# Kernel optimization log

Hardware: AMD Instinct MI355X
Metric: run time of the kernel (lower is better)

The kernel has to match this reference:

```python
import jax, jax.numpy as jnp
import numpy as np

B, S, HID, H, HKV, HD = 2, 1024, 4096, 32, 8, 128
NEG = -1e9
W_STD = 0.02


def _rotary(q, k, pos):
    # NeoX-style rotate-half rotary embedding, theta=10000
    inv_freq = 1.0 / (10000.0 ** (jnp.arange(0, HD, 2, dtype=jnp.float32) / HD))  # [HD/2]
    ang = pos[..., None].astype(jnp.float32) * inv_freq            # [B,S,HD/2]
    cos = jnp.concatenate([jnp.cos(ang), jnp.cos(ang)], -1)[:, :, None, :]  # [B,S,1,HD]
    sin = jnp.concatenate([jnp.sin(ang), jnp.sin(ang)], -1)[:, :, None, :]

    def rot_half(t):
        h1, h2 = jnp.split(t, 2, axis=-1)
        return jnp.concatenate([-h2, h1], axis=-1)

    return q * cos + rot_half(q) * sin, k * cos + rot_half(k) * sin


def setup_inputs() -> dict:
    key = jax.random.key(0)
    ks = jax.random.split(key, 6)
    x = jax.random.normal(ks[0], (B * S, HID), jnp.float32)
    wq = jax.random.normal(ks[1], (HID, H * HD), jnp.float32) * W_STD
    wk = jax.random.normal(ks[2], (HID, HKV * HD), jnp.float32) * W_STD
    wv = jax.random.normal(ks[3], (HID, HKV * HD), jnp.float32) * W_STD
    wo = jax.random.normal(ks[4], (H * HD, HID), jnp.float32) * W_STD
    # additive causal mask (module uses is_causal=False and an explicit attn_mask)
    attn_mask = jnp.where(jnp.triu(jnp.ones((S, S), bool), 1), NEG, 0.0).astype(jnp.float32)
    return {
        "x": x,
        "attn_mask": attn_mask,
        "wq": wq, "wk": wk, "wv": wv, "wo": wo,
        "seqstarts": jnp.arange(B + 1, dtype=jnp.int32) * S,
        "kvstarts": jnp.arange(B + 1, dtype=jnp.int32) * S,
        "cachestarts": jnp.arange(B, dtype=jnp.int32) * S,
        "decoding_batches": 0,
        "start_pos": jnp.zeros((B,), jnp.int32),
        "max_seqlen": S,
        "max_kvlen": S,
        "first_seqlen": jnp.full((B,), S, jnp.int32),
        "kv_cache": jnp.zeros((1,), jnp.float32),
        "kv_scale": jnp.zeros((1,), jnp.float32),
    }


def reference(x, attn_mask, wq, wk, wv, wo, seqstarts, kvstarts, cachestarts,
              decoding_batches, start_pos, max_seqlen, max_kvlen, first_seqlen,
              kv_cache, kv_scale):
    # QKV projections on flattened ragged tokens (uniform seqlens -> dense [B,S])
    xq = (x @ wq).reshape(B, S, H, HD)
    xk = (x @ wk).reshape(B, S, HKV, HD)
    xv = (x @ wv).reshape(B, S, HKV, HD)
    pos = start_pos[:, None] + jnp.arange(S, dtype=jnp.int32)  # [B,S]
    xq, xk = _rotary(xq, xk, pos)
    # GQA: repeat kv heads (friendly_gqa path of key_value_cache, num_repeat=4)
    g = H // HKV
    k = jnp.repeat(xk, g, axis=2)  # [B,S,H,HD]
    v = jnp.repeat(xv, g, axis=2)
    scale = 1.0 / jnp.sqrt(jnp.float32(HD))
    scores = jnp.einsum('bqhd,bkhd->bhqk', xq, k) * scale + attn_mask  # [B,H,S,S]
    p = jax.nn.softmax(scores, axis=-1)
    attn = jnp.einsum('bhqk,bkhd->bqhd', p, v).reshape(B * S, H * HD)
    return attn @ wo
```

## Files before the change

kernel.cpp:

```cpp
#include <hip/hip_runtime.h>
#include <hip/hip_bf16.h>

#define B_    2
#define S_    1024
#define HID_  4096
#define H_    32
#define HKV_  8
#define HD_   128

typedef __attribute__((ext_vector_type(8))) short   bf16x8_t;
typedef __attribute__((ext_vector_type(4))) float   f32x4_t;

__device__ __forceinline__ unsigned short f2bf(float f) {
    union { float f; unsigned u; } v; v.f = f;
    unsigned r = v.u + 0x7fffu + ((v.u >> 16) & 1u);
    return (unsigned short)(r >> 16);
}
__device__ __forceinline__ float bf2f(unsigned short u) {
    union { unsigned u; float f; } v; v.u = ((unsigned)u) << 16;
    return v.f;
}

__device__ __forceinline__ void gload_lds16(const void* g, void* l) {
    __builtin_amdgcn_global_load_lds(
        (const __attribute__((address_space(1))) unsigned int*)g,
        (__attribute__((address_space(3))) unsigned int*)l, 16, 0, 0);
}

__global__ __launch_bounds__(256) void cvt_f32_bf16(const float* __restrict__ in,
                                                    unsigned short* __restrict__ out,
                                                    int n4) {
    int i = blockIdx.x * 256 + threadIdx.x;
    if (i >= n4) return;
    float4 v = reinterpret_cast<const float4*>(in)[i];
    uint2 p;
    p.x = (unsigned)f2bf(v.x) | ((unsigned)f2bf(v.y) << 16);
    p.y = (unsigned)f2bf(v.z) | ((unsigned)f2bf(v.w) << 16);
    reinterpret_cast<uint2*>(out)[i] = p;
}

__global__ __launch_bounds__(256) void tcvt(const float* __restrict__ W,
                                            unsigned short* __restrict__ Wt,
                                            int ldW, int Kdim) {
    __shared__ unsigned short L[32][36];
    const int t = threadIdx.x;
    const int kb = blockIdx.y, nb = blockIdx.x;
    {
        int kr = t >> 3, nc = (t & 7) * 4;
        float4 v = *reinterpret_cast<const float4*>(&W[(size_t)(kb * 32 + kr) * ldW + nb * 32 + nc]);
        L[nc + 0][kr] = f2bf(v.x);
        L[nc + 1][kr] = f2bf(v.y);
        L[nc + 2][kr] = f2bf(v.z);
        L[nc + 3][kr] = f2bf(v.w);
    }
    __syncthreads();
    {
        int nr = t >> 3, kc = (t & 7) * 4;
        uint2 o;
        o.x = (unsigned)L[nr][kc + 0] | ((unsigned)L[nr][kc + 1] << 16);
        o.y = (unsigned)L[nr][kc + 2] | ((unsigned)L[nr][kc + 3] << 16);
        *reinterpret_cast<uint2*>(&Wt[(size_t)(nb * 32 + nr) * Kdim + kb * 32 + kc]) = o;
    }
}

template<bool OUT_BF16>
__global__ __launch_bounds__(256) void gemm_tt(
    const unsigned short* __restrict__ A,
    const unsigned short* __restrict__ Bt,
    void* __restrict__ Cm,
    int ldc, int K)
{
    __shared__ unsigned short As[2][128 * 32];
    __shared__ unsigned short Bs[2][128 * 32];
    const int tid  = threadIdx.x;
    const int lane = tid & 63;
    const int w    = tid >> 6;
    const int wm   = w >> 1, wn = w & 1;
    const int r    = lane & 15, g = lane >> 4;

    const int nwg = gridDim.x * gridDim.y;
    const int D   = blockIdx.y * gridDim.x + blockIdx.x;
    const int L   = (D & 7) * (nwg >> 3) + (D >> 3);
    const int m0  = (L / gridDim.x) * 128, n0 = (L % gridDim.x) * 128;

    const int c0 = w * 128 + lane;
    const int c1 = c0 + 64;
    const int r0 = c0 >> 2, col0 = (((c0 & 3) ^ (r0 & 3)) << 3);
    const int r1 = c1 >> 2, col1 = (((c1 & 3) ^ (r1 & 3)) << 3);
    const int sw = (g ^ (r & 3)) << 3;

    const f32x4_t zero = {0.f, 0.f, 0.f, 0.f};
    f32x4_t acc[4][4];
#pragma unroll
    for (int i = 0; i < 4; ++i)
#pragma unroll
        for (int j = 0; j < 4; ++j) acc[i][j] = zero;

    gload_lds16(&A [(size_t)(m0 + r0) * K + col0], &As[0][(w * 2 + 0) * 512]);
    gload_lds16(&A [(size_t)(m0 + r1) * K + col1], &As[0][(w * 2 + 1) * 512]);
    gload_lds16(&Bt[(size_t)(n0 + r0) * K + col0], &Bs[0][(w * 2 + 0) * 512]);
    gload_lds16(&Bt[(size_t)(n0 + r1) * K + col1], &Bs[0][(w * 2 + 1) * 512]);
    __syncthreads();

    int cur = 0;
    for (int k0 = 0; k0 < K; k0 += 32) {
        if (k0 + 32 < K) {
            const int nk = k0 + 32, nb = cur ^ 1;
            gload_lds16(&A [(size_t)(m0 + r0) * K + nk + col0], &As[nb][(w * 2 + 0) * 512]);
            gload_lds16(&A [(size_t)(m0 + r1) * K + nk + col1], &As[nb][(w * 2 + 1) * 512]);
            gload_lds16(&Bt[(size_t)(n0 + r0) * K + nk + col0], &Bs[nb][(w * 2 + 0) * 512]);
            gload_lds16(&Bt[(size_t)(n0 + r1) * K + nk + col1], &Bs[nb][(w * 2 + 1) * 512]);
        }
        bf16x8_t af[4], bfr[4];
#pragma unroll
        for (int m = 0; m < 4; ++m)
            af[m] = *reinterpret_cast<const bf16x8_t*>(&As[cur][(wm * 64 + m * 16 + r) * 32 + sw]);
#pragma unroll
        for (int n = 0; n < 4; ++n)
            bfr[n] = *reinterpret_cast<const bf16x8_t*>(&Bs[cur][(wn * 64 + n * 16 + r) * 32 + sw]);
#pragma unroll
        for (int m = 0; m < 4; ++m)
#pragma unroll
            for (int n = 0; n < 4; ++n)
                acc[m][n] = __builtin_amdgcn_mfma_f32_16x16x32_bf16(af[m], bfr[n], acc[m][n], 0, 0, 0);
        __syncthreads();
        cur ^= 1;
    }

#pragma unroll
    for (int m = 0; m < 4; ++m)
#pragma unroll
        for (int n = 0; n < 4; ++n)
#pragma unroll
            for (int j = 0; j < 4; ++j) {
                int row = m0 + wm * 64 + m * 16 + g * 4 + j;
                int col = n0 + wn * 64 + n * 16 + r;
                if constexpr (OUT_BF16)
                    reinterpret_cast<unsigned short*>(Cm)[(size_t)row * ldc + col] = f2bf(acc[m][n][j]);
                else
                    reinterpret_cast<float*>(Cm)[(size_t)row * ldc + col] = acc[m][n][j];
            }
}

__global__ __launch_bounds__(256) void gemm_qkv(
    const unsigned short* __restrict__ A,
    const unsigned short* __restrict__ BtQ,
    const unsigned short* __restrict__ BtKV,
    unsigned short* __restrict__ Qb,
    unsigned short* __restrict__ Kb,
    unsigned short* __restrict__ VT,
    int K)
{
    __shared__ unsigned short As[2][128 * 32];
    __shared__ unsigned short Bs[2][128 * 32];
    const int tid  = threadIdx.x;
    const int lane = tid & 63;
    const int w    = tid >> 6;
    const int wm   = w >> 1, wn = w & 1;
    const int r    = lane & 15, g = lane >> 4;

    const int nwg = gridDim.x * gridDim.y;
    const int D   = blockIdx.y * gridDim.x + blockIdx.x;
    const int L   = (D & 7) * (nwg >> 3) + (D >> 3);
    const int m0  = (L / gridDim.x) * 128, n0 = (L % gridDim.x) * 128;

    const unsigned short* Brow = (n0 < 4096) ? (BtQ + (size_t)n0 * K)
                                             : (BtKV + (size_t)(n0 - 4096) * K);

    const int c0 = w * 128 + lane;
    const int c1 = c0 + 64;
    const int r0 = c0 >> 2, col0 = (((c0 & 3) ^ (r0 & 3)) << 3);
    const int r1 = c1 >> 2, col1 = (((c1 & 3) ^ (r1 & 3)) << 3);
    const int sw = (g ^ (r & 3)) << 3;

    const f32x4_t zero = {0.f, 0.f, 0.f, 0.f};
    f32x4_t acc[4][4];
#pragma unroll
    for (int i = 0; i < 4; ++i)
#pragma unroll
        for (int j = 0; j < 4; ++j) acc[i][j] = zero;

    gload_lds16(&A   [(size_t)(m0 + r0) * K + col0], &As[0][(w * 2 + 0) * 512]);
    gload_lds16(&A   [(size_t)(m0 + r1) * K + col1], &As[0][(w * 2 + 1) * 512]);
    gload_lds16(&Brow[(size_t)r0 * K + col0],        &Bs[0][(w * 2 + 0) * 512]);
    gload_lds16(&Brow[(size_t)r1 * K + col1],        &Bs[0][(w * 2 + 1) * 512]);
    __syncthreads();

    int cur = 0;
    for (int k0 = 0; k0 < K; k0 += 32) {
        if (k0 + 32 < K) {
            const int nk = k0 + 32, nb = cur ^ 1;
            gload_lds16(&A   [(size_t)(m0 + r0) * K + nk + col0], &As[nb][(w * 2 + 0) * 512]);
            gload_lds16(&A   [(size_t)(m0 + r1) * K + nk + col1], &As[nb][(w * 2 + 1) * 512]);
            gload_lds16(&Brow[(size_t)r0 * K + nk + col0],        &Bs[nb][(w * 2 + 0) * 512]);
            gload_lds16(&Brow[(size_t)r1 * K + nk + col1],        &Bs[nb][(w * 2 + 1) * 512]);
        }
        bf16x8_t af[4], bfr[4];
#pragma unroll
        for (int m = 0; m < 4; ++m)
            af[m] = *reinterpret_cast<const bf16x8_t*>(&As[cur][(wm * 64 + m * 16 + r) * 32 + sw]);
#pragma unroll
        for (int n = 0; n < 4; ++n)
            bfr[n] = *reinterpret_cast<const bf16x8_t*>(&Bs[cur][(wn * 64 + n * 16 + r) * 32 + sw]);
#pragma unroll
        for (int m = 0; m < 4; ++m)
#pragma unroll
            for (int n = 0; n < 4; ++n)
                acc[m][n] = __builtin_amdgcn_mfma_f32_16x16x32_bf16(af[m], bfr[n], acc[m][n], 0, 0, 0);
        __syncthreads();
        cur ^= 1;
    }

#pragma unroll
    for (int m = 0; m < 4; ++m)
#pragma unroll
        for (int n = 0; n < 4; ++n) {
            int col  = n0 + wn * 64 + n * 16 + r;
            int row0 = m0 + wm * 64 + m * 16 + g * 4;
            if (n0 < 4096) {
#pragma unroll
                for (int j = 0; j < 4; ++j)
                    Qb[(size_t)(row0 + j) * 4096 + col] = f2bf(acc[m][n][j]);
            } else if (n0 < 5120) {
#pragma unroll
                for (int j = 0; j < 4; ++j)
                    Kb[(size_t)(row0 + j) * 1024 + (col - 4096)] = f2bf(acc[m][n][j]);
            } else {
                int d = col - 5120;
                int b = row0 >> 10, tokl = row0 & 1023;
                uint2 o;
                o.x = (unsigned)f2bf(acc[m][n][0]) | ((unsigned)f2bf(acc[m][n][1]) << 16);
                o.y = (unsigned)f2bf(acc[m][n][2]) | ((unsigned)f2bf(acc[m][n][3]) << 16);
                *reinterpret_cast<uint2*>(&VT[(size_t)(b * 1024 + d) * 1024 + tokl]) = o;
            }
        }
}

__global__ __launch_bounds__(256) void rope_table_kernel(const int* __restrict__ start_pos,
                                                         float* __restrict__ tab) {
    int i = blockIdx.x * 256 + threadIdx.x;
    int d = i & 63;
    int tok = i >> 6;
    int s = tok & (S_ - 1);
    int b = tok >> 10;
    float pos = (float)(start_pos[b] + s);
    float freq = __expf(-(float)d * (9.210340371976184f / 64.f));
    float ang = pos * freq;
    tab[tok * 128 + d]      = cosf(ang);
    tab[tok * 128 + 64 + d] = sinf(ang);
}

template<int LOGH, int STRIDE>
__global__ __launch_bounds__(256) void rope_apply_kernel(unsigned short* __restrict__ t,
                                                         const float* __restrict__ tab) {
    int i = blockIdx.x * 256 + threadIdx.x;
    int d = i & 63;
    int h = (i >> 6) & ((1 << LOGH) - 1);
    int tok = i >> (6 + LOGH);
    size_t base = (size_t)tok * STRIDE + (size_t)h * 128;
    float c  = tab[tok * 128 + d];
    float sn = tab[tok * 128 + 64 + d];
    float a = bf2f(t[base + d]);
    float b = bf2f(t[base + 64 + d]);
    t[base + d]      = f2bf(a * c - b * sn);
    t[base + 64 + d] = f2bf(b * c + a * sn);
}

__global__ __launch_bounds__(64) void attn_fwd(
    const unsigned short* __restrict__ Qb,
    const unsigned short* __restrict__ Kb,
    const unsigned short* __restrict__ VT,
    unsigned short* __restrict__ Ob)
{
    const int nQT = S_ / 32;
    const int qt = nQT - 1 - blockIdx.y;
    const int h = blockIdx.x, b = blockIdx.z;
    const int kvh = h >> 2;
    const int lane = threadIdx.x;
    const int r = lane & 15, g = lane >> 4;
    __shared__ unsigned short P_lds[32][40];

    const int qrow0 = qt * 32;
    const unsigned short* Qp = Qb + ((size_t)(b * S_) + qrow0) * 4096 + h * 128;
    bf16x8_t qf[2][4];
#pragma unroll
    for (int q2 = 0; q2 < 2; ++q2)
#pragma unroll
        for (int kk = 0; kk < 4; ++kk)
            qf[q2][kk] = *reinterpret_cast<const bf16x8_t*>(
                &Qp[(size_t)(q2 * 16 + r) * 4096 + kk * 32 + g * 8]);

    const f32x4_t zero = {0.f, 0.f, 0.f, 0.f};
    f32x4_t o[2][8];
#pragma unroll
    for (int q2 = 0; q2 < 2; ++q2)
#pragma unroll
        for (int n = 0; n < 8; ++n) o[q2][n] = zero;
    float m_[2][4], s_[2][4];
#pragma unroll
    for (int q2 = 0; q2 < 2; ++q2)
#pragma unroll
        for (int j = 0; j < 4; ++j) { m_[q2][j] = -1e30f; s_[q2][j] = 0.f; }

    const float scale = 0.08838834764831845f;
    const unsigned short* Kp = Kb + (size_t)(b * S_) * 1024 + kvh * 128;
    const unsigned short* Vt = VT + ((size_t)(b * 1024) + kvh * 128) * 1024;
    const int ntiles = qt + 1;

    for (int t = 0; t < ntiles; ++t) {
        const int k0 = t << 5;
        f32x4_t sc[2][2];
        sc[0][0] = zero; sc[0][1] = zero; sc[1][0] = zero; sc[1][1] = zero;
        __builtin_amdgcn_s_setprio(1);
#pragma unroll
        for (int kk = 0; kk < 4; ++kk) {
            bf16x8_t kf0 = *reinterpret_cast<const bf16x8_t*>(
                &Kp[(size_t)(k0 + r) * 1024 + kk * 32 + g * 8]);
            bf16x8_t kf1 = *reinterpret_cast<const bf16x8_t*>(
                &Kp[(size_t)(k0 + 16 + r) * 1024 + kk * 32 + g * 8]);
#pragma unroll
            for (int q2 = 0; q2 < 2; ++q2) {
                sc[q2][0] = __builtin_amdgcn_mfma_f32_16x16x32_bf16(qf[q2][kk], kf0, sc[q2][0], 0, 0, 0);
                sc[q2][1] = __builtin_amdgcn_mfma_f32_16x16x32_bf16(qf[q2][kk], kf1, sc[q2][1], 0, 0, 0);
            }
        }
        __builtin_amdgcn_s_setprio(0);
        bf16x8_t vf[8];
#pragma unroll
        for (int n = 0; n < 8; ++n)
            vf[n] = *reinterpret_cast<const bf16x8_t*>(
                &Vt[(size_t)(n * 16 + r) * 1024 + k0 + g * 8]);
        float al[2][4];
#pragma unroll
        for (int q2 = 0; q2 < 2; ++q2)
#pragma unroll
            for (int j = 0; j < 4; ++j) {
                int row = qrow0 + q2 * 16 + g * 4 + j;
                float v0 = sc[q2][0][j] * scale + ((k0 + r)      > row ? -1e9f : 0.f);
                float v1 = sc[q2][1][j] * scale + ((k0 + 16 + r) > row ? -1e9f : 0.f);
                float mx = fmaxf(v0, v1);
#pragma unroll
                for (int off = 1; off < 16; off <<= 1)
                    mx = fmaxf(mx, __shfl_xor(mx, off));
                float mn = fmaxf(m_[q2][j], mx);
                al[q2][j] = __expf(m_[q2][j] - mn);
                float p0 = __expf(v0 - mn);
                float p1 = __expf(v1 - mn);
                float rs = p0 + p1;
#pragma unroll
                for (int off = 1; off < 16; off <<= 1)
                    rs += __shfl_xor(rs, off);
                s_[q2][j] = s_[q2][j] * al[q2][j] + rs;
                m_[q2][j] = mn;
                P_lds[q2 * 16 + g * 4 + j][r]      = f2bf(p0);
                P_lds[q2 * 16 + g * 4 + j][16 + r] = f2bf(p1);
            }
#pragma unroll
        for (int q2 = 0; q2 < 2; ++q2)
#pragma unroll
            for (int n = 0; n < 8; ++n)
#pragma unroll
                for (int j = 0; j < 4; ++j)
                    o[q2][n][j] *= al[q2][j];
        __syncthreads();
        bf16x8_t pa[2];
        pa[0] = *reinterpret_cast<const bf16x8_t*>(&P_lds[r][g * 8]);
        pa[1] = *reinterpret_cast<const bf16x8_t*>(&P_lds[16 + r][g * 8]);
        __builtin_amdgcn_s_setprio(1);
#pragma unroll
        for (int n = 0; n < 8; ++n)
#pragma unroll
            for (int q2 = 0; q2 < 2; ++q2)
                o[q2][n] = __builtin_amdgcn_mfma_f32_16x16x32_bf16(pa[q2], vf[n], o[q2][n], 0, 0, 0);
        __builtin_amdgcn_s_setprio(0);
        __syncthreads();
    }
    unsigned short* Op = Ob + ((size_t)(b * S_) + qrow0) * 4096 + h * 128;
#pragma unroll
    for (int q2 = 0; q2 < 2; ++q2)
#pragma unroll
        for (int n = 0; n < 8; ++n)
#pragma unroll
            for (int j = 0; j < 4; ++j) {
                float val = o[q2][n][j] / s_[q2][j];
                Op[(size_t)(q2 * 16 + g * 4 + j) * 4096 + n * 16 + r] = f2bf(val);
            }
}

extern "C" void kernel_launch(void* const* d_in, const int* in_sizes, int n_in,
                              void* d_out, int out_size, void* d_ws, size_t ws_size,
                              hipStream_t stream)
{
    const float* x  = (const float*)d_in[0];
    const float* wq = (const float*)d_in[2];
    const float* wk = (const float*)d_in[3];
    const float* wv = (const float*)d_in[4];
    const float* wo = (const float*)d_in[5];
    const int* start_pos = (const int*)d_in[10];

    char* ws = (char*)d_ws;
    unsigned short* xb   = (unsigned short*)(ws);
    unsigned short* qb   = (unsigned short*)(ws + (16u << 20));
    unsigned short* kb   = (unsigned short*)(ws + (32u << 20));
    unsigned short* vT   = (unsigned short*)(ws + (36u << 20));
    unsigned short* wkvT = (unsigned short*)(ws + (40u << 20));
    float*          tb   = (float*)(ws + (56u << 20));
    unsigned short* ab   = xb;
    unsigned short* wqT  = (unsigned short*)d_out;
    unsigned short* woT  = qb;

    cvt_f32_bf16<<<8192, 256, 0, stream>>>(x, xb, (B_ * S_ * HID_) / 4);

    tcvt<<<dim3(128, 128), 256, 0, stream>>>(wq, wqT, HID_, HID_);
    tcvt<<<dim3(32, 128), 256, 0, stream>>>(wk, wkvT, 1024, HID_);
    tcvt<<<dim3(32, 128), 256, 0, stream>>>(wv, wkvT + (size_t)1024 * HID_, 1024, HID_);

    gemm_qkv<<<dim3(48, 16), 256, 0, stream>>>(xb, wqT, wkvT, qb, kb, vT, HID_);

    rope_table_kernel<<<512, 256, 0, stream>>>(start_pos, tb);
    rope_apply_kernel<5, 4096><<<16384, 256, 0, stream>>>(qb, tb);
    rope_apply_kernel<3, 1024><<<4096, 256, 0, stream>>>(kb, tb);

    attn_fwd<<<dim3(H_, S_ / 32, B_), 64, 0, stream>>>(qb, kb, vT, ab);

    tcvt<<<dim3(128, 128), 256, 0, stream>>>(wo, woT, HID_, HID_);
    gemm_tt<false><<<dim3(32, 16), 256, 0, stream>>>(ab, woT, (float*)d_out, 4096, HID_);
}
```

Measured before the change: 566.8 us.

## Fuse prep conversions, fold RoPE into QKV epilogue, merge attention with wo transpose

```diff
diff --git a/kernel.cpp b/kernel.cpp
--- a/kernel.cpp
+++ b/kernel.cpp
@@ -27,24 +27,10 @@
         (__attribute__((address_space(3))) unsigned int*)l, 16, 0, 0);
 }
 
-__global__ __launch_bounds__(256) void cvt_f32_bf16(const float* __restrict__ in,
-                                                    unsigned short* __restrict__ out,
-                                                    int n4) {
-    int i = blockIdx.x * 256 + threadIdx.x;
-    if (i >= n4) return;
-    float4 v = reinterpret_cast<const float4*>(in)[i];
-    uint2 p;
-    p.x = (unsigned)f2bf(v.x) | ((unsigned)f2bf(v.y) << 16);
-    p.y = (unsigned)f2bf(v.z) | ((unsigned)f2bf(v.w) << 16);
-    reinterpret_cast<uint2*>(out)[i] = p;
-}
-
-__global__ __launch_bounds__(256) void tcvt(const float* __restrict__ W,
-                                            unsigned short* __restrict__ Wt,
-                                            int ldW, int Kdim) {
-    __shared__ unsigned short L[32][36];
-    const int t = threadIdx.x;
-    const int kb = blockIdx.y, nb = blockIdx.x;
+__device__ __forceinline__ void tcvt_body(const float* __restrict__ W,
+                                          unsigned short* __restrict__ Wt,
+                                          int ldW, int nb, int kb,
+                                          unsigned short (*L)[36], int t) {
     {
         int kr = t >> 3, nc = (t & 7) * 4;
         float4 v = *reinterpret_cast<const float4*>(&W[(size_t)(kb * 32 + kr) * ldW + nb * 32 + nc]);
@@ -59,15 +45,300 @@
         uint2 o;
         o.x = (unsigned)L[nr][kc + 0] | ((unsigned)L[nr][kc + 1] << 16);
         o.y = (unsigned)L[nr][kc + 2] | ((unsigned)L[nr][kc + 3] << 16);
-        *reinterpret_cast<uint2*>(&Wt[(size_t)(nb * 32 + nr) * Kdim + kb * 32 + kc]) = o;
-    }
-}
-
-template<bool OUT_BF16>
+        *reinterpret_cast<uint2*>(&Wt[(size_t)(nb * 32 + nr) * 4096 + kb * 32 + kc]) = o;
+    }
+}
+
+__global__ __launch_bounds__(256) void prep(
+    const float* __restrict__ x,  const float* __restrict__ wq,
+    const float* __restrict__ wk, const float* __restrict__ wv,
+    const int* __restrict__ start_pos,
+    unsigned short* __restrict__ xb, unsigned short* __restrict__ wqT,
+    unsigned short* __restrict__ wkvT, float* __restrict__ tb)
+{
+    const int bid = blockIdx.x;
+    const int t   = threadIdx.x;
+    if (bid < 8192) {
+        int i = bid * 256 + t;
+        float4 v = reinterpret_cast<const float4*>(x)[i];
+        uint2 p;
+        p.x = (unsigned)f2bf(v.x) | ((unsigned)f2bf(v.y) << 16);
+        p.y = (unsigned)f2bf(v.z) | ((unsigned)f2bf(v.w) << 16);
+        reinterpret_cast<uint2*>(xb)[i] = p;
+        return;
+    }
+    if (bid >= 32768) {
+        int i = (bid - 32768) * 256 + t;
+        int d = i & 63;
+        int tok = i >> 6;
+        int s = tok & (S_ - 1);
+        int b = tok >> 10;
+        float pos = (float)(start_pos[b] + s);
+        float freq = __expf(-(float)d * (9.210340371976184f / 64.f));
+        float ang = pos * freq;
+        tb[tok * 128 + d]      = cosf(ang);
+        tb[tok * 128 + 64 + d] = sinf(ang);
+        return;
+    }
+    __shared__ unsigned short L[32][36];
+    if (bid < 24576) {
+        int q = bid - 8192;
+        tcvt_body(wq, wqT, 4096, q & 127, q >> 7, L, t);
+    } else if (bid < 28672) {
+        int q = bid - 24576;
+        tcvt_body(wk, wkvT, 1024, q & 31, q >> 5, L, t);
+    } else {
+        int q = bid - 28672;
+        tcvt_body(wv, wkvT + (size_t)1024 * 4096, 1024, q & 31, q >> 5, L, t);
+    }
+}
+
+__global__ __launch_bounds__(256) void gemm_qkv(
+    const unsigned short* __restrict__ A,
+    const unsigned short* __restrict__ BtQ,
+    const unsigned short* __restrict__ BtKV,
+    const float* __restrict__ tb,
+    unsigned short* __restrict__ Qb,
+    unsigned short* __restrict__ Kb,
+    unsigned short* __restrict__ VT,
+    int K)
+{
+    __shared__ unsigned short LDS[16384];
+    unsigned short* As0 = LDS;
+    unsigned short* Bs0 = LDS + 8192;
+    const int tid  = threadIdx.x;
+    const int lane = tid & 63;
+    const int w    = tid >> 6;
+    const int wm   = w >> 1, wn = w & 1;
+    const int r    = lane & 15, g = lane >> 4;
+
+    const int nwg = gridDim.x * gridDim.y;
+    const int D   = blockIdx.y * gridDim.x + blockIdx.x;
+    const int L   = (D & 7) * (nwg >> 3) + (D >> 3);
+    const int m0  = (L / gridDim.x) * 128, n0 = (L % gridDim.x) * 128;
+
+    const unsigned short* Brow = (n0 < 4096) ? (BtQ + (size_t)n0 * K)
+                                             : (BtKV + (size_t)(n0 - 4096) * K);
+
+    const int c0 = w * 128 + lane;
+    const int c1 = c0 + 64;
+    const int r0 = c0 >> 2, col0 = (((c0 & 3) ^ (r0 & 3)) << 3);
+    const int r1 = c1 >> 2, col1 = (((c1 & 3) ^ (r1 & 3)) << 3);
+    const int sw = (g ^ (r & 3)) << 3;
+
+    const f32x4_t zero = {0.f, 0.f, 0.f, 0.f};
+    f32x4_t acc[4][4];
+#pragma unroll
+    for (int i = 0; i < 4; ++i)
+#pragma unroll
+        for (int j = 0; j < 4; ++j) acc[i][j] = zero;
+
+    gload_lds16(&A   [(size_t)(m0 + r0) * K + col0], &As0[(w * 2 + 0) * 512]);
+    gload_lds16(&A   [(size_t)(m0 + r1) * K + col1], &As0[(w * 2 + 1) * 512]);
+    gload_lds16(&Brow[(size_t)r0 * K + col0],        &Bs0[(w * 2 + 0) * 512]);
+    gload_lds16(&Brow[(size_t)r1 * K + col1],        &Bs0[(w * 2 + 1) * 512]);
+    __syncthreads();
+
+    int cur = 0;
+    for (int k0 = 0; k0 < K; k0 += 32) {
+        if (k0 + 32 < K) {
+            const int nk = k0 + 32, nb = cur ^ 1;
+            gload_lds16(&A   [(size_t)(m0 + r0) * K + nk + col0], &As0[nb * 4096 + (w * 2 + 0) * 512]);
+            gload_lds16(&A   [(size_t)(m0 + r1) * K + nk + col1], &As0[nb * 4096 + (w * 2 + 1) * 512]);
+            gload_lds16(&Brow[(size_t)r0 * K + nk + col0],        &Bs0[nb * 4096 + (w * 2 + 0) * 512]);
+            gload_lds16(&Brow[(size_t)r1 * K + nk + col1],        &Bs0[nb * 4096 + (w * 2 + 1) * 512]);
+        }
+        bf16x8_t af[4], bfr[4];
+#pragma unroll
+        for (int m = 0; m < 4; ++m)
+            af[m] = *reinterpret_cast<const bf16x8_t*>(&As0[cur * 4096 + (wm * 64 + m * 16 + r) * 32 + sw]);
+#pragma unroll
+        for (int n = 0; n < 4; ++n)
+            bfr[n] = *reinterpret_cast<const bf16x8_t*>(&Bs0[cur * 4096 + (wn * 64 + n * 16 + r) * 32 + sw]);
+#pragma unroll
+        for (int m = 0; m < 4; ++m)
+#pragma unroll
+            for (int n = 0; n < 4; ++n)
+                acc[m][n] = __builtin_amdgcn_mfma_f32_16x16x32_bf16(af[m], bfr[n], acc[m][n], 0, 0, 0);
+        __syncthreads();
+        cur ^= 1;
+    }
+
+    if (n0 < 5120) {
+#pragma unroll
+        for (int m = 0; m < 4; ++m)
+#pragma unroll
+            for (int n = 0; n < 4; ++n)
+#pragma unroll
+                for (int j = 0; j < 4; ++j)
+                    LDS[(wm * 64 + m * 16 + g * 4 + j) * 128 + wn * 64 + n * 16 + r] = f2bf(acc[m][n][j]);
+        __syncthreads();
+        unsigned short* dst; int ldd, coff;
+        if (n0 < 4096) { dst = Qb; ldd = 4096; coff = n0; }
+        else           { dst = Kb; ldd = 1024; coff = n0 - 4096; }
+        for (int i = tid; i < 8192; i += 256) {
+            int row = i >> 6, dlo = i & 63;
+            int tok = m0 + row;
+            float a  = bf2f(LDS[row * 128 + dlo]);
+            float b  = bf2f(LDS[row * 128 + 64 + dlo]);
+            float c  = tb[tok * 128 + dlo];
+            float sn = tb[tok * 128 + 64 + dlo];
+            dst[(size_t)tok * ldd + coff + dlo]      = f2bf(a * c - b * sn);
+            dst[(size_t)tok * ldd + coff + 64 + dlo] = f2bf(b * c + a * sn);
+        }
+    } else {
+#pragma unroll
+        for (int m = 0; m < 4; ++m)
+#pragma unroll
+            for (int n = 0; n < 4; ++n) {
+                int col  = n0 + wn * 64 + n * 16 + r;
+                int row0 = m0 + wm * 64 + m * 16 + g * 4;
+                int d = col - 5120;
+                int b = row0 >> 10, tokl = row0 & 1023;
+                uint2 o;
+                o.x = (unsigned)f2bf(acc[m][n][0]) | ((unsigned)f2bf(acc[m][n][1]) << 16);
+                o.y = (unsigned)f2bf(acc[m][n][2]) | ((unsigned)f2bf(acc[m][n][3]) << 16);
+                *reinterpret_cast<uint2*>(&VT[(size_t)(b * 1024 + d) * 1024 + tokl]) = o;
+            }
+    }
+}
+
+__global__ __launch_bounds__(256) void attn_tcvt(
+    unsigned short* __restrict__ Qb,
+    const unsigned short* __restrict__ Kb,
+    const unsigned short* __restrict__ VT,
+    const float* __restrict__ wo,
+    unsigned short* __restrict__ woT)
+{
+    const int bid = blockIdx.x;
+    const int tid = threadIdx.x;
+    __shared__ unsigned short P_lds[4][32][40];
+    __shared__ unsigned short Lt[32][36];
+
+    if (bid >= 512) {
+        int q = bid - 512;
+        tcvt_body(wo, woT, 4096, q & 127, q >> 7, Lt, tid);
+        return;
+    }
+
+    const int wid  = tid >> 6;
+    const int lane = tid & 63;
+    const int h    = bid & 31;
+    const int tmp  = bid >> 5;
+    const int qtg  = tmp & 7;
+    const int b    = tmp >> 3;
+    const int qt   = 31 - (qtg + wid * 8);
+    const int kvh  = h >> 2;
+    const int r = lane & 15, g = lane >> 4;
+
+    const int qrow0 = qt * 32;
+    unsigned short* Qp = Qb + ((size_t)(b * S_) + qrow0) * 4096 + h * 128;
+    bf16x8_t qf[2][4];
+#pragma unroll
+    for (int q2 = 0; q2 < 2; ++q2)
+#pragma unroll
+        for (int kk = 0; kk < 4; ++kk)
+            qf[q2][kk] = *reinterpret_cast<const bf16x8_t*>(
+                &Qp[(size_t)(q2 * 16 + r) * 4096 + kk * 32 + g * 8]);
+
+    const f32x4_t zero = {0.f, 0.f, 0.f, 0.f};
+    f32x4_t o[2][8];
+#pragma unroll
+    for (int q2 = 0; q2 < 2; ++q2)
+#pragma unroll
+        for (int n = 0; n < 8; ++n) o[q2][n] = zero;
+    float m_[2][4], s_[2][4];
+#pragma unroll
+    for (int q2 = 0; q2 < 2; ++q2)
+#pragma unroll
+        for (int j = 0; j < 4; ++j) { m_[q2][j] = -1e30f; s_[q2][j] = 0.f; }
+
+    const float scale = 0.08838834764831845f;
+    const unsigned short* Kp = Kb + (size_t)(b * S_) * 1024 + kvh * 128;
+    const unsigned short* Vt = VT + ((size_t)(b * 1024) + kvh * 128) * 1024;
+    const int ntiles = qt + 1;
+
+    for (int t = 0; t < ntiles; ++t) {
+        const int k0 = t << 5;
+        f32x4_t sc[2][2];
+        sc[0][0] = zero; sc[0][1] = zero; sc[1][0] = zero; sc[1][1] = zero;
+        __builtin_amdgcn_s_setprio(1);
+#pragma unroll
+        for (int kk = 0; kk < 4; ++kk) {
+            bf16x8_t kf0 = *reinterpret_cast<const bf16x8_t*>(
+                &Kp[(size_t)(k0 + r) * 1024 + kk * 32 + g * 8]);
+            bf16x8_t kf1 = *reinterpret_cast<const bf16x8_t*>(
+                &Kp[(size_t)(k0 + 16 + r) * 1024 + kk * 32 + g * 8]);
+#pragma unroll
+            for (int q2 = 0; q2 < 2; ++q2) {
+                sc[q2][0] = __builtin_amdgcn_mfma_f32_16x16x32_bf16(qf[q2][kk], kf0, sc[q2][0], 0, 0, 0);
+                sc[q2][1] = __builtin_amdgcn_mfma_f32_16x16x32_bf16(qf[q2][kk], kf1, sc[q2][1], 0, 0, 0);
+            }
+        }
+        __builtin_amdgcn_s_setprio(0);
+        bf16x8_t vf[8];
+#pragma unroll
+        for (int n = 0; n < 8; ++n)
+            vf[n] = *reinterpret_cast<const bf16x8_t*>(
+                &Vt[(size_t)(n * 16 + r) * 1024 + k0 + g * 8]);
+        float al[2][4];
+#pragma unroll
+        for (int q2 = 0; q2 < 2; ++q2)
+#pragma unroll
+            for (int j = 0; j < 4; ++j) {
+                int row = qrow0 + q2 * 16 + g * 4 + j;
+                float v0 = sc[q2][0][j] * scale + ((k0 + r)      > row ? -1e9f : 0.f);
+                float v1 = sc[q2][1][j] * scale + ((k0 + 16 + r) > row ? -1e9f : 0.f);
+                float mx = fmaxf(v0, v1);
+#pragma unroll
+                for (int off = 1; off < 16; off <<= 1)
+                    mx = fmaxf(mx, __shfl_xor(mx, off));
+                float mn = fmaxf(m_[q2][j], mx);
+                al[q2][j] = __expf(m_[q2][j] - mn);
+                float p0 = __expf(v0 - mn);
+                float p1 = __expf(v1 - mn);
+                float rs = p0 + p1;
+#pragma unroll
+                for (int off = 1; off < 16; off <<= 1)
+                    rs += __shfl_xor(rs, off);
+                s_[q2][j] = s_[q2][j] * al[q2][j] + rs;
+                m_[q2][j] = mn;
+                P_lds[wid][q2 * 16 + g * 4 + j][r]      = f2bf(p0);
+                P_lds[wid][q2 * 16 + g * 4 + j][16 + r] = f2bf(p1);
+            }
+#pragma unroll
+        for (int q2 = 0; q2 < 2; ++q2)
+#pragma unroll
+            for (int n = 0; n < 8; ++n)
+#pragma unroll
+                for (int j = 0; j < 4; ++j)
+                    o[q2][n][j] *= al[q2][j];
+        bf16x8_t pa[2];
+        pa[0] = *reinterpret_cast<const bf16x8_t*>(&P_lds[wid][r][g * 8]);
+        pa[1] = *reinterpret_cast<const bf16x8_t*>(&P_lds[wid][16 + r][g * 8]);
+        __builtin_amdgcn_s_setprio(1);
+#pragma unroll
+        for (int n = 0; n < 8; ++n)
+#pragma unroll
+            for (int q2 = 0; q2 < 2; ++q2)
+                o[q2][n] = __builtin_amdgcn_mfma_f32_16x16x32_bf16(pa[q2], vf[n], o[q2][n], 0, 0, 0);
+        __builtin_amdgcn_s_setprio(0);
+    }
+#pragma unroll
+    for (int q2 = 0; q2 < 2; ++q2)
+#pragma unroll
+        for (int n = 0; n < 8; ++n)
+#pragma unroll
+            for (int j = 0; j < 4; ++j) {
+                float val = o[q2][n][j] / s_[q2][j];
+                Qp[(size_t)(q2 * 16 + g * 4 + j) * 4096 + n * 16 + r] = f2bf(val);
+            }
+}
+
 __global__ __launch_bounds__(256) void gemm_tt(
     const unsigned short* __restrict__ A,
     const unsigned short* __restrict__ Bt,
-    void* __restrict__ Cm,
+    float* __restrict__ Cm,
     int ldc, int K)
 {
     __shared__ unsigned short As[2][128 * 32];
@@ -135,255 +406,7 @@
             for (int j = 0; j < 4; ++j) {
                 int row = m0 + wm * 64 + m * 16 + g * 4 + j;
                 int col = n0 + wn * 64 + n * 16 + r;
-                if constexpr (OUT_BF16)
-                    reinterpret_cast<unsigned short*>(Cm)[(size_t)row * ldc + col] = f2bf(acc[m][n][j]);
-                else
-                    reinterpret_cast<float*>(Cm)[(size_t)row * ldc + col] = acc[m][n][j];
-            }
-}
-
-__global__ __launch_bounds__(256) void gemm_qkv(
-    const unsigned short* __restrict__ A,
-    const unsigned short* __restrict__ BtQ,
-    const unsigned short* __restrict__ BtKV,
-    unsigned short* __restrict__ Qb,
-    unsigned short* __restrict__ Kb,
-    unsigned short* __restrict__ VT,
-    int K)
-{
-    __shared__ unsigned short As[2][128 * 32];
-    __shared__ unsigned short Bs[2][128 * 32];
-    const int tid  = threadIdx.x;
-    const int lane = tid & 63;
-    const int w    = tid >> 6;
-    const int wm   = w >> 1, wn = w & 1;
-    const int r    = lane & 15, g = lane >> 4;
-
-    const int nwg = gridDim.x * gridDim.y;
-    const int D   = blockIdx.y * gridDim.x + blockIdx.x;
-    const int L   = (D & 7) * (nwg >> 3) + (D >> 3);
-    const int m0  = (L / gridDim.x) * 128, n0 = (L % gridDim.x) * 128;
-
-    const unsigned short* Brow = (n0 < 4096) ? (BtQ + (size_t)n0 * K)
-                                             : (BtKV + (size_t)(n0 - 4096) * K);
-
-    const int c0 = w * 128 + lane;
-    const int c1 = c0 + 64;
-    const int r0 = c0 >> 2, col0 = (((c0 & 3) ^ (r0 & 3)) << 3);
-    const int r1 = c1 >> 2, col1 = (((c1 & 3) ^ (r1 & 3)) << 3);
-    const int sw = (g ^ (r & 3)) << 3;
-
-    const f32x4_t zero = {0.f, 0.f, 0.f, 0.f};
-    f32x4_t acc[4][4];
-#pragma unroll
-    for (int i = 0; i < 4; ++i)
-#pragma unroll
-        for (int j = 0; j < 4; ++j) acc[i][j] = zero;
-
-    gload_lds16(&A   [(size_t)(m0 + r0) * K + col0], &As[0][(w * 2 + 0) * 512]);
-    gload_lds16(&A   [(size_t)(m0 + r1) * K + col1], &As[0][(w * 2 + 1) * 512]);
-    gload_lds16(&Brow[(size_t)r0 * K + col0],        &Bs[0][(w * 2 + 0) * 512]);
-    gload_lds16(&Brow[(size_t)r1 * K + col1],        &Bs[0][(w * 2 + 1) * 512]);
-    __syncthreads();
-
-    int cur = 0;
-    for (int k0 = 0; k0 < K; k0 += 32) {
-        if (k0 + 32 < K) {
-            const int nk = k0 + 32, nb = cur ^ 1;
-            gload_lds16(&A   [(size_t)(m0 + r0) * K + nk + col0], &As[nb][(w * 2 + 0) * 512]);
-            gload_lds16(&A   [(size_t)(m0 + r1) * K + nk + col1], &As[nb][(w * 2 + 1) * 512]);
-            gload_lds16(&Brow[(size_t)r0 * K + nk + col0],        &Bs[nb][(w * 2 + 0) * 512]);
-            gload_lds16(&Brow[(size_t)r1 * K + nk + col1],        &Bs[nb][(w * 2 + 1) * 512]);
-        }
-        bf16x8_t af[4], bfr[4];
-#pragma unroll
-        for (int m = 0; m < 4; ++m)
-            af[m] = *reinterpret_cast<const bf16x8_t*>(&As[cur][(wm * 64 + m * 16 + r) * 32 + sw]);
-#pragma unroll
-        for (int n = 0; n < 4; ++n)
-            bfr[n] = *reinterpret_cast<const bf16x8_t*>(&Bs[cur][(wn * 64 + n * 16 + r) * 32 + sw]);
-#pragma unroll
-        for (int m = 0; m < 4; ++m)
-#pragma unroll
-            for (int n = 0; n < 4; ++n)
-                acc[m][n] = __builtin_amdgcn_mfma_f32_16x16x32_bf16(af[m], bfr[n], acc[m][n], 0, 0, 0);
-        __syncthreads();
-        cur ^= 1;
-    }
-
-#pragma unroll
-    for (int m = 0; m < 4; ++m)
-#pragma unroll
-        for (int n = 0; n < 4; ++n) {
-            int col  = n0 + wn * 64 + n * 16 + r;
-            int row0 = m0 + wm * 64 + m * 16 + g * 4;
-            if (n0 < 4096) {
-#pragma unroll
-                for (int j = 0; j < 4; ++j)
-                    Qb[(size_t)(row0 + j) * 4096 + col] = f2bf(acc[m][n][j]);
-            } else if (n0 < 5120) {
-#pragma unroll
-                for (int j = 0; j < 4; ++j)
-                    Kb[(size_t)(row0 + j) * 1024 + (col - 4096)] = f2bf(acc[m][n][j]);
-            } else {
-                int d = col - 5120;
-                int b = row0 >> 10, tokl = row0 & 1023;
-                uint2 o;
-                o.x = (unsigned)f2bf(acc[m][n][0]) | ((unsigned)f2bf(acc[m][n][1]) << 16);
-                o.y = (unsigned)f2bf(acc[m][n][2]) | ((unsigned)f2bf(acc[m][n][3]) << 16);
-                *reinterpret_cast<uint2*>(&VT[(size_t)(b * 1024 + d) * 1024 + tokl]) = o;
-            }
-        }
-}
-
-__global__ __launch_bounds__(256) void rope_table_kernel(const int* __restrict__ start_pos,
-                                                         float* __restrict__ tab) {
-    int i = blockIdx.x * 256 + threadIdx.x;
-    int d = i & 63;
-    int tok = i >> 6;
-    int s = tok & (S_ - 1);
-    int b = tok >> 10;
-    float pos = (float)(start_pos[b] + s);
-    float freq = __expf(-(float)d * (9.210340371976184f / 64.f));
-    float ang = pos * freq;
-    tab[tok * 128 + d]      = cosf(ang);
-    tab[tok * 128 + 64 + d] = sinf(ang);
-}
-
-template<int LOGH, int STRIDE>
-__global__ __launch_bounds__(256) void rope_apply_kernel(unsigned short* __restrict__ t,
-                                                         const float* __restrict__ tab) {
-    int i = blockIdx.x * 256 + threadIdx.x;
-    int d = i & 63;
-    int h = (i >> 6) & ((1 << LOGH) - 1);
-    int tok = i >> (6 + LOGH);
-    size_t base = (size_t)tok * STRIDE + (size_t)h * 128;
-    float c  = tab[tok * 128 + d];
-    float sn = tab[tok * 128 + 64 + d];
-    float a = bf2f(t[base + d]);
-    float b = bf2f(t[base + 64 + d]);
-    t[base + d]      = f2bf(a * c - b * sn);
-    t[base + 64 + d] = f2bf(b * c + a * sn);
-}
-
-__global__ __launch_bounds__(64) void attn_fwd(
-    const unsigned short* __restrict__ Qb,
-    const unsigned short* __restrict__ Kb,
-    const unsigned short* __restrict__ VT,
-    unsigned short* __restrict__ Ob)
-{
-    const int nQT = S_ / 32;
-    const int qt = nQT - 1 - blockIdx.y;
-    const int h = blockIdx.x, b = blockIdx.z;
-    const int kvh = h >> 2;
-    const int lane = threadIdx.x;
-    const int r = lane & 15, g = lane >> 4;
-    __shared__ unsigned short P_lds[32][40];
-
-    const int qrow0 = qt * 32;
-    const unsigned short* Qp = Qb + ((size_t)(b * S_) + qrow0) * 4096 + h * 128;
-    bf16x8_t qf[2][4];
-#pragma unroll
-    for (int q2 = 0; q2 < 2; ++q2)
-#pragma unroll
-        for (int kk = 0; kk < 4; ++kk)
-            qf[q2][kk] = *reinterpret_cast<const bf16x8_t*>(
-                &Qp[(size_t)(q2 * 16 + r) * 4096 + kk * 32 + g * 8]);
-
-    const f32x4_t zero = {0.f, 0.f, 0.f, 0.f};
-    f32x4_t o[2][8];
-#pragma unroll
-    for (int q2 = 0; q2 < 2; ++q2)
-#pragma unroll
-        for (int n = 0; n < 8; ++n) o[q2][n] = zero;
-    float m_[2][4], s_[2][4];
-#pragma unroll
-    for (int q2 = 0; q2 < 2; ++q2)
-#pragma unroll
-        for (int j = 0; j < 4; ++j) { m_[q2][j] = -1e30f; s_[q2][j] = 0.f; }
-
-    const float scale = 0.08838834764831845f;
-    const unsigned short* Kp = Kb + (size_t)(b * S_) * 1024 + kvh * 128;
-    const unsigned short* Vt = VT + ((size_t)(b * 1024) + kvh * 128) * 1024;
-    const int ntiles = qt + 1;
-
-    for (int t = 0; t < ntiles; ++t) {
-        const int k0 = t << 5;
-        f32x4_t sc[2][2];
-        sc[0][0] = zero; sc[0][1] = zero; sc[1][0] = zero; sc[1][1] = zero;
-        __builtin_amdgcn_s_setprio(1);
-#pragma unroll
-        for (int kk = 0; kk < 4; ++kk) {
-            bf16x8_t kf0 = *reinterpret_cast<const bf16x8_t*>(
-                &Kp[(size_t)(k0 + r) * 1024 + kk * 32 + g * 8]);
-            bf16x8_t kf1 = *reinterpret_cast<const bf16x8_t*>(
-                &Kp[(size_t)(k0 + 16 + r) * 1024 + kk * 32 + g * 8]);
-#pragma unroll
-            for (int q2 = 0; q2 < 2; ++q2) {
-                sc[q2][0] = __builtin_amdgcn_mfma_f32_16x16x32_bf16(qf[q2][kk], kf0, sc[q2][0], 0, 0, 0);
-                sc[q2][1] = __builtin_amdgcn_mfma_f32_16x16x32_bf16(qf[q2][kk], kf1, sc[q2][1], 0, 0, 0);
-            }
-        }
-        __builtin_amdgcn_s_setprio(0);
-        bf16x8_t vf[8];
-#pragma unroll
-        for (int n = 0; n < 8; ++n)
-            vf[n] = *reinterpret_cast<const bf16x8_t*>(
-                &Vt[(size_t)(n * 16 + r) * 1024 + k0 + g * 8]);
-        float al[2][4];
-#pragma unroll
-        for (int q2 = 0; q2 < 2; ++q2)
-#pragma unroll
-            for (int j = 0; j < 4; ++j) {
-                int row = qrow0 + q2 * 16 + g * 4 + j;
-                float v0 = sc[q2][0][j] * scale + ((k0 + r)      > row ? -1e9f : 0.f);
-                float v1 = sc[q2][1][j] * scale + ((k0 + 16 + r) > row ? -1e9f : 0.f);
-                float mx = fmaxf(v0, v1);
-#pragma unroll
-                for (int off = 1; off < 16; off <<= 1)
-                    mx = fmaxf(mx, __shfl_xor(mx, off));
-                float mn = fmaxf(m_[q2][j], mx);
-                al[q2][j] = __expf(m_[q2][j] - mn);
-                float p0 = __expf(v0 - mn);
-                float p1 = __expf(v1 - mn);
-                float rs = p0 + p1;
-#pragma unroll
-                for (int off = 1; off < 16; off <<= 1)
-                    rs += __shfl_xor(rs, off);
-                s_[q2][j] = s_[q2][j] * al[q2][j] + rs;
-                m_[q2][j] = mn;
-                P_lds[q2 * 16 + g * 4 + j][r]      = f2bf(p0);
-                P_lds[q2 * 16 + g * 4 + j][16 + r] = f2bf(p1);
-            }
-#pragma unroll
-        for (int q2 = 0; q2 < 2; ++q2)
-#pragma unroll
-            for (int n = 0; n < 8; ++n)
-#pragma unroll
-                for (int j = 0; j < 4; ++j)
-                    o[q2][n][j] *= al[q2][j];
-        __syncthreads();
-        bf16x8_t pa[2];
-        pa[0] = *reinterpret_cast<const bf16x8_t*>(&P_lds[r][g * 8]);
-        pa[1] = *reinterpret_cast<const bf16x8_t*>(&P_lds[16 + r][g * 8]);
-        __builtin_amdgcn_s_setprio(1);
-#pragma unroll
-        for (int n = 0; n < 8; ++n)
-#pragma unroll
-            for (int q2 = 0; q2 < 2; ++q2)
-                o[q2][n] = __builtin_amdgcn_mfma_f32_16x16x32_bf16(pa[q2], vf[n], o[q2][n], 0, 0, 0);
-        __builtin_amdgcn_s_setprio(0);
-        __syncthreads();
-    }
-    unsigned short* Op = Ob + ((size_t)(b * S_) + qrow0) * 4096 + h * 128;
-#pragma unroll
-    for (int q2 = 0; q2 < 2; ++q2)
-#pragma unroll
-        for (int n = 0; n < 8; ++n)
-#pragma unroll
-            for (int j = 0; j < 4; ++j) {
-                float val = o[q2][n][j] / s_[q2][j];
-                Op[(size_t)(q2 * 16 + g * 4 + j) * 4096 + n * 16 + r] = f2bf(val);
+                Cm[(size_t)row * ldc + col] = acc[m][n][j];
             }
 }
 
@@ -399,30 +422,20 @@
     const int* start_pos = (const int*)d_in[10];
 
     char* ws = (char*)d_ws;
-    unsigned short* xb   = (unsigned short*)(ws);
-    unsigned short* qb   = (unsigned short*)(ws + (16u << 20));
-    unsigned short* kb   = (unsigned short*)(ws + (32u << 20));
-    unsigned short* vT   = (unsigned short*)(ws + (36u << 20));
+    unsigned short* qb   = (unsigned short*)(ws);
+    unsigned short* kb   = (unsigned short*)(ws + (16u << 20));
+    unsigned short* vT   = (unsigned short*)(ws + (20u << 20));
+    unsigned short* xb   = (unsigned short*)(ws + (24u << 20));
     unsigned short* wkvT = (unsigned short*)(ws + (40u << 20));
     float*          tb   = (float*)(ws + (56u << 20));
-    unsigned short* ab   = xb;
     unsigned short* wqT  = (unsigned short*)d_out;
-    unsigned short* woT  = qb;
-
-    cvt_f32_bf16<<<8192, 256, 0, stream>>>(x, xb, (B_ * S_ * HID_) / 4);
-
-    tcvt<<<dim3(128, 128), 256, 0, stream>>>(wq, wqT, HID_, HID_);
-    tcvt<<<dim3(32, 128), 256, 0, stream>>>(wk, wkvT, 1024, HID_);
-    tcvt<<<dim3(32, 128), 256, 0, stream>>>(wv, wkvT + (size_t)1024 * HID_, 1024, HID_);
-
-    gemm_qkv<<<dim3(48, 16), 256, 0, stream>>>(xb, wqT, wkvT, qb, kb, vT, HID_);
-
-    rope_table_kernel<<<512, 256, 0, stream>>>(start_pos, tb);
-    rope_apply_kernel<5, 4096><<<16384, 256, 0, stream>>>(qb, tb);
-    rope_apply_kernel<3, 1024><<<4096, 256, 0, stream>>>(kb, tb);
-
-    attn_fwd<<<dim3(H_, S_ / 32, B_), 64, 0, stream>>>(qb, kb, vT, ab);
-
-    tcvt<<<dim3(128, 128), 256, 0, stream>>>(wo, woT, HID_, HID_);
-    gemm_tt<false><<<dim3(32, 16), 256, 0, stream>>>(ab, woT, (float*)d_out, 4096, HID_);
-}
+    unsigned short* woT  = xb;
+
+    prep<<<33280, 256, 0, stream>>>(x, wq, wk, wv, start_pos, xb, wqT, wkvT, tb);
+
+    gemm_qkv<<<dim3(48, 16), 256, 0, stream>>>(xb, wqT, wkvT, tb, qb, kb, vT, HID_);
+
+    attn_tcvt<<<512 + 16384, 256, 0, stream>>>(qb, kb, vT, wo, woT);
+
+    gemm_tt<<<dim3(32, 16), 256, 0, stream>>>(qb, woT, (float*)d_out, 4096, HID_);
+}
```

Measured after the change: 656.6 us. +15.8%, slower.
